# Performance work log

Measured on AMD Instinct MI355X. Metric: run time of the kernel, lower is better.

The kernel has to match this reference:

```python
import jax, jax.numpy as jnp
import numpy as np

EMBED_DIM = 1024
NUM_HEADS = 16
HEAD_DIM = EMBED_DIM // NUM_HEADS


def setup_inputs() -> dict:
    key = jax.random.key(0)
    ks = jax.random.split(key, 10)
    s = 1.0 / np.sqrt(EMBED_DIM)
    inp = {
        "x1": jax.random.normal(ks[0], (4, 1024, EMBED_DIM), jnp.float32),
        "x2": jax.random.normal(ks[1], (4, 2048, EMBED_DIM), jnp.float32),
        "Wq": jax.random.normal(ks[2], (EMBED_DIM, EMBED_DIM), jnp.float32) * s,
        "bq": jnp.zeros((EMBED_DIM,), jnp.float32),
        "Wk": jax.random.normal(ks[3], (EMBED_DIM, EMBED_DIM), jnp.float32) * s,
        "bk": jnp.zeros((EMBED_DIM,), jnp.float32),
        "Wv": jax.random.normal(ks[4], (EMBED_DIM, EMBED_DIM), jnp.float32) * s,
        "bv": jnp.zeros((EMBED_DIM,), jnp.float32),
        "Wo": jax.random.normal(ks[5], (EMBED_DIM, EMBED_DIM), jnp.float32) * s,
        "bo": jnp.zeros((EMBED_DIM,), jnp.float32),
    }
    return inp


def reference(x1, x2, Wq, bq, Wk, bk, Wv, bv, Wo, bo):
    B, Sq, E = x1.shape
    Skv = x2.shape[1]
    H, D = NUM_HEADS, HEAD_DIM
    # linear projections (PyTorch Linear: x @ W.T + b)
    q = (x1 @ Wq.T + bq).reshape(B, Sq, H, D).transpose(0, 2, 1, 3)   # [B,H,Sq,D]
    k = (x2 @ Wk.T + bk).reshape(B, Skv, H, D).transpose(0, 2, 1, 3)  # [B,H,Skv,D]
    v = (x2 @ Wv.T + bv).reshape(B, Skv, H, D).transpose(0, 2, 1, 3)
    scores = jnp.einsum("bhqd,bhkd->bhqk", q, k) / jnp.sqrt(jnp.float32(D))
    attn = jax.nn.softmax(scores, axis=-1)
    out = jnp.einsum("bhqk,bhkd->bhqd", attn, v)
    out = out.transpose(0, 2, 1, 3).reshape(B, Sq, E)
    return out @ Wo.T + bo
```

## Files before the change

### kernel.cpp

```cpp
#include <hip/hip_runtime.h>

typedef __attribute__((ext_vector_type(8))) short short8;
typedef __attribute__((ext_vector_type(4))) short short4v;
typedef __attribute__((ext_vector_type(4))) float f32x4;

#define ASYNC16(g, l) __builtin_amdgcn_global_load_lds( \
    (__attribute__((address_space(1))) void*)(g), \
    (__attribute__((address_space(3))) void*)(l), 16, 0, 0)

__device__ __forceinline__ short f2bf(float f) {
  union { float f; unsigned u; } v; v.f = f;
  unsigned r = v.u + 0x7fffu + ((v.u >> 16) & 1u);
  return (short)(r >> 16);
}

__device__ __forceinline__ unsigned pack_bf2(float lo, float hi) {
  union { float f; unsigned u; } a, b; a.f = lo; b.f = hi;
  return __builtin_amdgcn_perm(b.u + 0x8000u, a.u + 0x8000u, 0x07060302u);
}

__device__ __forceinline__ f32x4 fzero4() {
  f32x4 z; z[0] = 0.f; z[1] = 0.f; z[2] = 0.f; z[3] = 0.f; return z;
}

__device__ __forceinline__ void wg_barrier() {
  asm volatile("s_waitcnt lgkmcnt(0)\n\ts_barrier" ::: "memory");
}

__global__ __launch_bounds__(256) void cvt_all(
    const float* __restrict__ x1, const float* __restrict__ x2,
    const float* __restrict__ wq, const float* __restrict__ wk,
    const float* __restrict__ wv, const float* __restrict__ wo,
    short* __restrict__ dst) {
  long e = ((long)blockIdx.x * 256 + threadIdx.x) * 4;
  const float* src; long loc;
  if (e < 4194304L)       { src = x1; loc = e; }
  else if (e < 12582912L) { src = x2; loc = e - 4194304L; }
  else if (e < 13631488L) { src = wq; loc = e - 12582912L; }
  else if (e < 14680064L) { src = wk; loc = e - 13631488L; }
  else if (e < 15728640L) { src = wv; loc = e - 14680064L; }
  else                    { src = wo; loc = e - 15728640L; }
  float4 v = *(const float4*)(src + loc);
  short4v o;
  o[0] = f2bf(v.x); o[1] = f2bf(v.y); o[2] = f2bf(v.z); o[3] = f2bf(v.w);
  *(short4v*)(dst + e) = o;
}

__global__ __launch_bounds__(256) void proj(
    const short* __restrict__ xb1, const short* __restrict__ xb2,
    const short* __restrict__ wqp, const short* __restrict__ wkp, const short* __restrict__ wvp,
    const float* __restrict__ bq, const float* __restrict__ bk, const float* __restrict__ bv,
    short* __restrict__ qb, short* __restrict__ kb, short* __restrict__ vb) {
  __shared__ short smem[16384];
  short* As = smem;
  short* Bs = smem + 4096;
  const int tid = threadIdx.x, w = tid >> 6, lane = tid & 63;
  const int quad = lane >> 4, col = lane & 15;
  const int waveM = (w >> 1) * 64, waveN = (w & 1) * 64;
  const int my = blockIdx.x, bn = blockIdx.y * 128;
  const short* A; const short* W; const float* bias; int mode, bm;
  if (my < 32)      { A = xb1; W = wqp; bias = bq; mode = 0; bm = my * 128; }
  else if (my < 96) { A = xb2; W = wkp; bias = bk; mode = 1; bm = (my - 32) * 128; }
  else              { A = xb2; W = wvp; bias = bv; mode = 2; bm = (my - 96) * 128; }

  f32x4 acc[4][4];
  for (int mi = 0; mi < 4; ++mi)
    for (int ni = 0; ni < 4; ++ni)
      acc[mi][ni] = fzero4();

  const int srow = w * 16 + (lane >> 2), scol = (lane & 3) * 8;
  const short* ga = A + (size_t)(bm + srow) * 1024 + scol;
  const short* gb = W + (size_t)(bn + srow) * 1024 + scol;
  short* lA = As + w * 512;
  short* lB = Bs + w * 512;

  for (int kk = 0; kk < 1024; kk += 32) {
    __syncthreads();
    ASYNC16(ga + kk,         lA);
    ASYNC16(ga + kk + 65536, lA + 2048);
    ASYNC16(gb + kk,         lB);
    ASYNC16(gb + kk + 65536, lB + 2048);
    __syncthreads();
    short8 af[4], bf[4];
    for (int mi = 0; mi < 4; ++mi)
      af[mi] = *(const short8*)(As + (waveM + mi * 16 + col) * 32 + quad * 8);
    for (int ni = 0; ni < 4; ++ni)
      bf[ni] = *(const short8*)(Bs + (waveN + ni * 16 + col) * 32 + quad * 8);
    for (int mi = 0; mi < 4; ++mi)
      for (int ni = 0; ni < 4; ++ni)
        acc[mi][ni] = __builtin_amdgcn_mfma_f32_16x16x32_bf16(af[mi], bf[ni], acc[mi][ni], 0, 0, 0);
  }

  __syncthreads();
  for (int ni = 0; ni < 4; ++ni) {
    int nn = waveN + ni * 16 + col;
    float bvl = bias[bn + nn];
    for (int mi = 0; mi < 4; ++mi) {
      int m0 = waveM + mi * 16 + quad * 4;
      for (int r = 0; r < 4; ++r) {
        int m = m0 + r;
        smem[m * 128 + (nn ^ ((m & 15) << 3))] = f2bf(acc[mi][ni][r] + bvl);
      }
    }
  }
  __syncthreads();
  if (mode < 2) {
    const int S = (mode == 0) ? 1024 : 2048;
    short* outp = (mode == 0) ? qb : kb;
    const int bb = bm / S, s0 = bm & (S - 1), h0 = bn >> 6;
    for (int it = 0; it < 8; ++it) {
      int f = (it * 256 + tid) * 8;
      int hh = f >> 13, rem = f & 8191, m = rem >> 6, d = rem & 63;
      int nn = hh * 64 + d;
      short8 val = *(const short8*)&smem[m * 128 + (nn ^ ((m & 15) << 3))];
      *(short8*)(outp + ((((size_t)(bb * 16 + h0 + hh)) * S + s0 + m) * 64 + d)) = val;
    }
  } else {
    const int bb = bm >> 11, s0 = bm & 2047, kt0 = s0 >> 6, h0 = bn >> 6;
    for (int it = 0; it < 8; ++it) {
      int f = (it * 256 + tid) * 8;
      int hh = f >> 13, rem = f & 8191, ktl = rem >> 12, r3 = rem & 4095;
      int d = r3 >> 6, kvp0 = r3 & 63;
      int nn = hh * 64 + d;
      short8 val;
      for (int j = 0; j < 8; ++j) {
        int kvp = kvp0 + j;
        int kv = ((kvp & 3) << 4) | (kvp >> 2);
        int m = ktl * 64 + kv;
        val[j] = smem[m * 128 + (nn ^ ((m & 15) << 3))];
      }
      *(short8*)(vb + ((((size_t)(bb * 16 + h0 + hh)) * 32 + (kt0 + ktl)) * 4096) + d * 64 + kvp0) = val;
    }
  }
}

__global__ __launch_bounds__(256) void out_gemm(
    const short* __restrict__ A, const short* __restrict__ W,
    const float* __restrict__ bias, float* __restrict__ out) {
  __shared__ short As[64 * 32];
  __shared__ short Bs[128 * 32];
  const int tid = threadIdx.x, w = tid >> 6, lane = tid & 63;
  const int quad = lane >> 4, col = lane & 15;
  const int waveM = (w >> 1) * 32, waveN = (w & 1) * 64;
  const int bn = blockIdx.x * 128, bm = blockIdx.y * 64;

  f32x4 acc[2][4];
  for (int mi = 0; mi < 2; ++mi)
    for (int ni = 0; ni < 4; ++ni)
      acc[mi][ni] = fzero4();

  const short* ga = A + (size_t)(bm + (tid >> 2)) * 1024 + (tid & 3) * 8;
  const short* gb = W + (size_t)(bn + (tid >> 2)) * 1024 + (tid & 3) * 8;
  short* lA = As + w * 512;
  short* lB = Bs + w * 512;

  for (int kk = 0; kk < 1024; kk += 32) {
    __syncthreads();
    ASYNC16(ga + kk,         lA);
    ASYNC16(gb + kk,         lB);
    ASYNC16(gb + kk + 65536, lB + 2048);
    __syncthreads();
    short8 af[2], bf[4];
    for (int mi = 0; mi < 2; ++mi)
      af[mi] = *(const short8*)(As + (waveM + mi * 16 + col) * 32 + quad * 8);
    for (int ni = 0; ni < 4; ++ni)
      bf[ni] = *(const short8*)(Bs + (waveN + ni * 16 + col) * 32 + quad * 8);
    for (int mi = 0; mi < 2; ++mi)
      for (int ni = 0; ni < 4; ++ni)
        acc[mi][ni] = __builtin_amdgcn_mfma_f32_16x16x32_bf16(af[mi], bf[ni], acc[mi][ni], 0, 0, 0);
  }

  for (int ni = 0; ni < 4; ++ni) {
    int n = bn + waveN + ni * 16 + col;
    float bvl = bias[n];
    for (int mi = 0; mi < 2; ++mi) {
      int m0 = bm + waveM + mi * 16 + quad * 4;
      for (int r = 0; r < 4; ++r)
        out[(size_t)(m0 + r) * 1024 + n] = acc[mi][ni][r] + bvl;
    }
  }
}

__global__ __launch_bounds__(256, 2) void attn(
    const short* __restrict__ Q, const short* __restrict__ K,
    const short* __restrict__ V, short* __restrict__ O) {
  __shared__ short Ks[128 * 72];
  __shared__ short Vs[64 * 136];
  __shared__ short Ps[128 * 136];
  const int tid = threadIdx.x, w = tid >> 6, lane = tid & 63;
  const int quad = lane >> 4, col = lane & 15;
  const int bh = blockIdx.x, qt = blockIdx.y;
  const int b = bh >> 4, h = bh & 15;
  const int qbase = w * 32;

  const short* qp = Q + ((size_t)bh * 1024 + qt * 128) * 64;
  const short* kp = K + (size_t)bh * 131072;
  const short* vp = V + (size_t)bh * 131072;

  short8 aq[2][2];
  for (int mi = 0; mi < 2; ++mi) {
    const short* qr = qp + (qbase + mi * 16 + col) * 64 + quad * 8;
    aq[mi][0] = *(const short8*)qr;
    aq[mi][1] = *(const short8*)(qr + 32);
  }

  float lsum[2][4];
  f32x4 oa[2][4];
  for (int mi = 0; mi < 2; ++mi) {
    for (int r = 0; r < 4; ++r) lsum[mi][r] = 0.f;
    for (int ni = 0; ni < 4; ++ni) oa[mi][ni] = fzero4();
  }

  const int krow = lane + (w >> 1) * 64, kch = (w & 1) * 32;
  const int vd = lane, vch = w & 1, vkh = (w >> 1) * 32;
  const float c = 0.18033688011112042f;

  short8 kpre[4], vpre[4];
  {
    const short* kg = kp + krow * 64 + kch;
    const short* vg = vp + vch * 4096 + vd * 64 + vkh;
    for (int i = 0; i < 4; ++i) kpre[i] = *(const short8*)(kg + i * 8);
    for (int i = 0; i < 4; ++i) vpre[i] = *(const short8*)(vg + i * 8);
  }

  for (int kt = 0; kt < 16; ++kt) {
    wg_barrier();
    for (int i = 0; i < 4; ++i)
      *(short8*)&Ks[krow * 72 + kch + i * 8] = kpre[i];
    for (int i = 0; i < 4; ++i)
      *(short8*)&Vs[vd * 136 + vch * 64 + vkh + i * 8] = vpre[i];
    {
      int ktn = (kt < 15) ? kt + 1 : kt;
      const short* kg = kp + ktn * 8192 + krow * 64 + kch;
      const short* vg = vp + (2 * ktn + vch) * 4096 + vd * 64 + vkh;
      for (int i = 0; i < 4; ++i) kpre[i] = *(const short8*)(kg + i * 8);
      for (int i = 0; i < 4; ++i) vpre[i] = *(const short8*)(vg + i * 8);
    }
    wg_barrier();

    for (int mi = 0; mi < 2; ++mi) {
      f32x4 sf[8];
      for (int nk = 0; nk < 8; ++nk) {
        short8 bk0 = *(const short8*)&Ks[(nk * 16 + col) * 72 + quad * 8];
        short8 bk1 = *(const short8*)&Ks[(nk * 16 + col) * 72 + 32 + quad * 8];
        f32x4 z = fzero4();
        z = __builtin_amdgcn_mfma_f32_16x16x32_bf16(aq[mi][0], bk0, z, 0, 0, 0);
        z = __builtin_amdgcn_mfma_f32_16x16x32_bf16(aq[mi][1], bk1, z, 0, 0, 0);
        sf[nk] = z;
      }
      for (int nk = 0; nk < 8; ++nk)
        for (int r = 0; r < 4; ++r)
          sf[nk][r] = __builtin_amdgcn_exp2f(sf[nk][r] * c);
      for (int r = 0; r < 4; ++r)
        lsum[mi][r] += ((sf[0][r] + sf[1][r]) + (sf[2][r] + sf[3][r])) +
                       ((sf[4][r] + sf[5][r]) + (sf[6][r] + sf[7][r]));
      for (int r = 0; r < 4; ++r) {
        int row = qbase + mi * 16 + quad * 4 + r;
        uint2 d0, d1;
        d0.x = pack_bf2(sf[0][r], sf[1][r]);
        d0.y = pack_bf2(sf[2][r], sf[3][r]);
        d1.x = pack_bf2(sf[4][r], sf[5][r]);
        d1.y = pack_bf2(sf[6][r], sf[7][r]);
        *(uint2*)&Ps[row * 136 + col * 4]      = d0;
        *(uint2*)&Ps[row * 136 + 64 + col * 4] = d1;
      }
    }

    for (int ks = 0; ks < 4; ++ks) {
      int koff = ks * 32 + quad * 8;
      short8 ap0 = *(const short8*)&Ps[(qbase + col) * 136 + koff];
      short8 ap1 = *(const short8*)&Ps[(qbase + 16 + col) * 136 + koff];
      for (int ni = 0; ni < 4; ++ni) {
        short8 bv = *(const short8*)&Vs[(ni * 16 + col) * 136 + koff];
        oa[0][ni] = __builtin_amdgcn_mfma_f32_16x16x32_bf16(ap0, bv, oa[0][ni], 0, 0, 0);
        oa[1][ni] = __builtin_amdgcn_mfma_f32_16x16x32_bf16(ap1, bv, oa[1][ni], 0, 0, 0);
      }
    }
  }

  for (int mi = 0; mi < 2; ++mi)
    for (int r = 0; r < 4; ++r) {
      float s = lsum[mi][r];
      s += __shfl_xor(s, 1);
      s += __shfl_xor(s, 2);
      s += __shfl_xor(s, 4);
      s += __shfl_xor(s, 8);
      lsum[mi][r] = 1.f / s;
    }
  __syncthreads();
  for (int mi = 0; mi < 2; ++mi)
    for (int ni = 0; ni < 4; ++ni)
      for (int r = 0; r < 4; ++r)
        Ps[(qbase + mi * 16 + quad * 4 + r) * 64 + ni * 16 + col] = f2bf(oa[mi][ni][r] * lsum[mi][r]);
  __syncthreads();
  for (int it = 0; it < 4; ++it) {
    int f = (it * 256 + tid) * 8;
    int q = f >> 6, d = f & 63;
    short8 val = *(const short8*)&Ps[q * 64 + d];
    *(short8*)(O + ((size_t)(b * 1024 + qt * 128 + q)) * 1024 + h * 64 + d) = val;
  }
}

extern "C" void kernel_launch(void* const* d_in, const int* in_sizes, int n_in,
                              void* d_out, int out_size, void* d_ws, size_t ws_size,
                              hipStream_t stream) {
  const float* x1 = (const float*)d_in[0];
  const float* x2 = (const float*)d_in[1];
  const float* Wq = (const float*)d_in[2];
  const float* bq = (const float*)d_in[3];
  const float* Wk = (const float*)d_in[4];
  const float* bk = (const float*)d_in[5];
  const float* Wv = (const float*)d_in[6];
  const float* bv = (const float*)d_in[7];
  const float* Wo = (const float*)d_in[8];
  const float* bo = (const float*)d_in[9];

  char* ws = (char*)d_ws;
  short* xb1 = (short*)(ws + 0);
  short* xb2 = (short*)(ws + 8388608);
  short* wqb = (short*)(ws + 25165824);
  short* wkb = (short*)(ws + 27262976);
  short* wvb = (short*)(ws + 29360128);
  short* wob = (short*)(ws + 31457280);
  short* qb  = (short*)(ws + 33554432);
  short* kb  = (short*)(ws + 41943040);
  short* vb  = (short*)(ws + 58720256);
  short* ob  = (short*)(ws + 75497472);

  cvt_all<<<16384, 256, 0, stream>>>(x1, x2, Wq, Wk, Wv, Wo, (short*)ws);
  proj<<<dim3(160, 8), 256, 0, stream>>>(xb1, xb2, wqb, wkb, wvb, bq, bk, bv, qb, kb, vb);
  attn<<<dim3(64, 8), 256, 0, stream>>>(qb, kb, vb, ob);
  out_gemm<<<dim3(8, 64), 256, 0, stream>>>(ob, wob, bo, (float*)d_out);
}
```

Baseline: 246.2 us.

## Fold softmax scale into Q, use fp16 P/V with row-sum MFMA column, retile out GEMM

```diff
diff --git a/kernel.cpp b/kernel.cpp
--- a/kernel.cpp
+++ b/kernel.cpp
@@ -3,6 +3,7 @@
 typedef __attribute__((ext_vector_type(8))) short short8;
 typedef __attribute__((ext_vector_type(4))) short short4v;
 typedef __attribute__((ext_vector_type(4))) float f32x4;
+typedef _Float16 half8 __attribute__((ext_vector_type(8)));
 
 #define ASYNC16(g, l) __builtin_amdgcn_global_load_lds( \
     (__attribute__((address_space(1))) void*)(g), \
@@ -14,9 +15,13 @@
   return (short)(r >> 16);
 }
 
-__device__ __forceinline__ unsigned pack_bf2(float lo, float hi) {
-  union { float f; unsigned u; } a, b; a.f = lo; b.f = hi;
-  return __builtin_amdgcn_perm(b.u + 0x8000u, a.u + 0x8000u, 0x07060302u);
+__device__ __forceinline__ short f2h(float f) {
+  _Float16 h = (_Float16)f;
+  return __builtin_bit_cast(short, h);
+}
+
+__device__ __forceinline__ unsigned pkh2(float a, float b) {
+  return __builtin_bit_cast(unsigned, __builtin_amdgcn_cvt_pkrtz(a, b));
 }
 
 __device__ __forceinline__ f32x4 fzero4() {
@@ -99,7 +104,12 @@
       int m0 = waveM + mi * 16 + quad * 4;
       for (int r = 0; r < 4; ++r) {
         int m = m0 + r;
-        smem[m * 128 + (nn ^ ((m & 15) << 3))] = f2bf(acc[mi][ni][r] + bvl);
+        float val = acc[mi][ni][r] + bvl;
+        short sv;
+        if (mode == 0)      sv = f2bf(val * 0.18033688011112042f);
+        else if (mode == 1) sv = f2bf(val);
+        else                sv = f2h(val);
+        smem[m * 128 + (nn ^ ((m & 15) << 3))] = sv;
       }
     }
   }
@@ -137,43 +147,51 @@
 __global__ __launch_bounds__(256) void out_gemm(
     const short* __restrict__ A, const short* __restrict__ W,
     const float* __restrict__ bias, float* __restrict__ out) {
-  __shared__ short As[64 * 32];
-  __shared__ short Bs[128 * 32];
+  __shared__ short As[2][4096];
+  __shared__ short Bs[2][2048];
   const int tid = threadIdx.x, w = tid >> 6, lane = tid & 63;
   const int quad = lane >> 4, col = lane & 15;
-  const int waveM = (w >> 1) * 32, waveN = (w & 1) * 64;
-  const int bn = blockIdx.x * 128, bm = blockIdx.y * 64;
-
-  f32x4 acc[2][4];
-  for (int mi = 0; mi < 2; ++mi)
-    for (int ni = 0; ni < 4; ++ni)
+  const int waveM = (w >> 1) * 64, waveN = (w & 1) * 32;
+  const int bn = blockIdx.x * 64, bm = blockIdx.y * 128;
+
+  f32x4 acc[4][2];
+  for (int mi = 0; mi < 4; ++mi)
+    for (int ni = 0; ni < 2; ++ni)
       acc[mi][ni] = fzero4();
 
-  const short* ga = A + (size_t)(bm + (tid >> 2)) * 1024 + (tid & 3) * 8;
+  const int arow = w * 16 + (lane >> 2), ac = (lane & 3) * 8;
+  const short* ga = A + (size_t)(bm + arow) * 1024 + ac;
   const short* gb = W + (size_t)(bn + (tid >> 2)) * 1024 + (tid & 3) * 8;
-  short* lA = As + w * 512;
-  short* lB = Bs + w * 512;
-
-  for (int kk = 0; kk < 1024; kk += 32) {
+  short* lA0 = As[0] + w * 512; short* lA1 = As[1] + w * 512;
+  short* lB0 = Bs[0] + w * 512; short* lB1 = Bs[1] + w * 512;
+
+  for (int kk = 0; kk < 1024; kk += 64) {
     __syncthreads();
-    ASYNC16(ga + kk,         lA);
-    ASYNC16(gb + kk,         lB);
-    ASYNC16(gb + kk + 65536, lB + 2048);
+    ASYNC16(ga + kk,              lA0);
+    ASYNC16(ga + kk + 65536,      lA0 + 2048);
+    ASYNC16(ga + kk + 32,         lA1);
+    ASYNC16(ga + kk + 32 + 65536, lA1 + 2048);
+    ASYNC16(gb + kk,              lB0);
+    ASYNC16(gb + kk + 32,         lB1);
     __syncthreads();
-    short8 af[2], bf[4];
-    for (int mi = 0; mi < 2; ++mi)
-      af[mi] = *(const short8*)(As + (waveM + mi * 16 + col) * 32 + quad * 8);
-    for (int ni = 0; ni < 4; ++ni)
-      bf[ni] = *(const short8*)(Bs + (waveN + ni * 16 + col) * 32 + quad * 8);
-    for (int mi = 0; mi < 2; ++mi)
-      for (int ni = 0; ni < 4; ++ni)
-        acc[mi][ni] = __builtin_amdgcn_mfma_f32_16x16x32_bf16(af[mi], bf[ni], acc[mi][ni], 0, 0, 0);
-  }
-
-  for (int ni = 0; ni < 4; ++ni) {
+    for (int kh = 0; kh < 2; ++kh) {
+      const short* Ash = As[kh];
+      const short* Bsh = Bs[kh];
+      short8 af[4], bf[2];
+      for (int mi = 0; mi < 4; ++mi)
+        af[mi] = *(const short8*)(Ash + (waveM + mi * 16 + col) * 32 + quad * 8);
+      for (int ni = 0; ni < 2; ++ni)
+        bf[ni] = *(const short8*)(Bsh + (waveN + ni * 16 + col) * 32 + quad * 8);
+      for (int mi = 0; mi < 4; ++mi)
+        for (int ni = 0; ni < 2; ++ni)
+          acc[mi][ni] = __builtin_amdgcn_mfma_f32_16x16x32_bf16(af[mi], bf[ni], acc[mi][ni], 0, 0, 0);
+    }
+  }
+
+  for (int ni = 0; ni < 2; ++ni) {
     int n = bn + waveN + ni * 16 + col;
     float bvl = bias[n];
-    for (int mi = 0; mi < 2; ++mi) {
+    for (int mi = 0; mi < 4; ++mi) {
       int m0 = bm + waveM + mi * 16 + quad * 4;
       for (int r = 0; r < 4; ++r)
         out[(size_t)(m0 + r) * 1024 + n] = acc[mi][ni][r] + bvl;
@@ -185,7 +203,7 @@
     const short* __restrict__ Q, const short* __restrict__ K,
     const short* __restrict__ V, short* __restrict__ O) {
   __shared__ short Ks[128 * 72];
-  __shared__ short Vs[64 * 136];
+  __shared__ short Vs[80 * 136];
   __shared__ short Ps[128 * 136];
   const int tid = threadIdx.x, w = tid >> 6, lane = tid & 63;
   const int quad = lane >> 4, col = lane & 15;
@@ -204,16 +222,16 @@
     aq[mi][1] = *(const short8*)(qr + 32);
   }
 
-  float lsum[2][4];
-  f32x4 oa[2][4];
-  for (int mi = 0; mi < 2; ++mi) {
-    for (int r = 0; r < 4; ++r) lsum[mi][r] = 0.f;
-    for (int ni = 0; ni < 4; ++ni) oa[mi][ni] = fzero4();
-  }
+  f32x4 oa[2][5];
+  for (int mi = 0; mi < 2; ++mi)
+    for (int ni = 0; ni < 5; ++ni)
+      oa[mi][ni] = fzero4();
+
+  for (int i = tid; i < 16 * 136; i += 256)
+    Vs[64 * 136 + i] = (i < 136) ? (short)0x3C00 : (short)0;
 
   const int krow = lane + (w >> 1) * 64, kch = (w & 1) * 32;
   const int vd = lane, vch = w & 1, vkh = (w >> 1) * 32;
-  const float c = 0.18033688011112042f;
 
   short8 kpre[4], vpre[4];
   {
@@ -238,60 +256,58 @@
     }
     wg_barrier();
 
-    for (int mi = 0; mi < 2; ++mi) {
-      f32x4 sf[8];
-      for (int nk = 0; nk < 8; ++nk) {
-        short8 bk0 = *(const short8*)&Ks[(nk * 16 + col) * 72 + quad * 8];
-        short8 bk1 = *(const short8*)&Ks[(nk * 16 + col) * 72 + 32 + quad * 8];
-        f32x4 z = fzero4();
-        z = __builtin_amdgcn_mfma_f32_16x16x32_bf16(aq[mi][0], bk0, z, 0, 0, 0);
-        z = __builtin_amdgcn_mfma_f32_16x16x32_bf16(aq[mi][1], bk1, z, 0, 0, 0);
-        sf[nk] = z;
-      }
+    f32x4 sf[2][8];
+    for (int nk = 0; nk < 8; ++nk) {
+      short8 bk0 = *(const short8*)&Ks[(nk * 16 + col) * 72 + quad * 8];
+      short8 bk1 = *(const short8*)&Ks[(nk * 16 + col) * 72 + 32 + quad * 8];
+      f32x4 z0 = fzero4(), z1 = fzero4();
+      z0 = __builtin_amdgcn_mfma_f32_16x16x32_bf16(aq[0][0], bk0, z0, 0, 0, 0);
+      z0 = __builtin_amdgcn_mfma_f32_16x16x32_bf16(aq[0][1], bk1, z0, 0, 0, 0);
+      z1 = __builtin_amdgcn_mfma_f32_16x16x32_bf16(aq[1][0], bk0, z1, 0, 0, 0);
+      z1 = __builtin_amdgcn_mfma_f32_16x16x32_bf16(aq[1][1], bk1, z1, 0, 0, 0);
+      sf[0][nk] = z0;
+      sf[1][nk] = z1;
+    }
+
+    for (int mi = 0; mi < 2; ++mi)
       for (int nk = 0; nk < 8; ++nk)
         for (int r = 0; r < 4; ++r)
-          sf[nk][r] = __builtin_amdgcn_exp2f(sf[nk][r] * c);
-      for (int r = 0; r < 4; ++r)
-        lsum[mi][r] += ((sf[0][r] + sf[1][r]) + (sf[2][r] + sf[3][r])) +
-                       ((sf[4][r] + sf[5][r]) + (sf[6][r] + sf[7][r]));
+          sf[mi][nk][r] = __builtin_amdgcn_exp2f(sf[mi][nk][r]);
+    for (int mi = 0; mi < 2; ++mi)
       for (int r = 0; r < 4; ++r) {
         int row = qbase + mi * 16 + quad * 4 + r;
         uint2 d0, d1;
-        d0.x = pack_bf2(sf[0][r], sf[1][r]);
-        d0.y = pack_bf2(sf[2][r], sf[3][r]);
-        d1.x = pack_bf2(sf[4][r], sf[5][r]);
-        d1.y = pack_bf2(sf[6][r], sf[7][r]);
+        d0.x = pkh2(sf[mi][0][r], sf[mi][1][r]);
+        d0.y = pkh2(sf[mi][2][r], sf[mi][3][r]);
+        d1.x = pkh2(sf[mi][4][r], sf[mi][5][r]);
+        d1.y = pkh2(sf[mi][6][r], sf[mi][7][r]);
         *(uint2*)&Ps[row * 136 + col * 4]      = d0;
         *(uint2*)&Ps[row * 136 + 64 + col * 4] = d1;
       }
-    }
 
     for (int ks = 0; ks < 4; ++ks) {
       int koff = ks * 32 + quad * 8;
-      short8 ap0 = *(const short8*)&Ps[(qbase + col) * 136 + koff];
-      short8 ap1 = *(const short8*)&Ps[(qbase + 16 + col) * 136 + koff];
-      for (int ni = 0; ni < 4; ++ni) {
-        short8 bv = *(const short8*)&Vs[(ni * 16 + col) * 136 + koff];
-        oa[0][ni] = __builtin_amdgcn_mfma_f32_16x16x32_bf16(ap0, bv, oa[0][ni], 0, 0, 0);
-        oa[1][ni] = __builtin_amdgcn_mfma_f32_16x16x32_bf16(ap1, bv, oa[1][ni], 0, 0, 0);
+      half8 ap0 = *(const half8*)&Ps[(qbase + col) * 136 + koff];
+      half8 ap1 = *(const half8*)&Ps[(qbase + 16 + col) * 136 + koff];
+      for (int ni = 0; ni < 5; ++ni) {
+        half8 bv = *(const half8*)&Vs[(ni * 16 + col) * 136 + koff];
+        oa[0][ni] = __builtin_amdgcn_mfma_f32_16x16x32_f16(ap0, bv, oa[0][ni], 0, 0, 0);
+        oa[1][ni] = __builtin_amdgcn_mfma_f32_16x16x32_f16(ap1, bv, oa[1][ni], 0, 0, 0);
       }
     }
   }
 
+  float inv[2][4];
   for (int mi = 0; mi < 2; ++mi)
     for (int r = 0; r < 4; ++r) {
-      float s = lsum[mi][r];
-      s += __shfl_xor(s, 1);
-      s += __shfl_xor(s, 2);
-      s += __shfl_xor(s, 4);
-      s += __shfl_xor(s, 8);
-      lsum[mi][r] = 1.f / s;
+      float s = __shfl(oa[mi][4][r], lane & 48);
+      inv[mi][r] = 1.f / s;
     }
   __syncthreads();
   for (int mi = 0; mi < 2; ++mi)
     for (int ni = 0; ni < 4; ++ni)
       for (int r = 0; r < 4; ++r)
-        Ps[(qbase + mi * 16 + quad * 4 + r) * 64 + ni * 16 + col] = f2bf(oa[mi][ni][r] * lsum[mi][r]);
+        Ps[(qbase + mi * 16 + quad * 4 + r) * 64 + ni * 16 + col] = f2bf(oa[mi][ni][r] * inv[mi][r]);
   __syncthreads();
   for (int it = 0; it < 4; ++it) {
     int f = (it * 256 + tid) * 8;
@@ -330,5 +346,5 @@
   cvt_all<<<16384, 256, 0, stream>>>(x1, x2, Wq, Wk, Wv, Wo, (short*)ws);
   proj<<<dim3(160, 8), 256, 0, stream>>>(xb1, xb2, wqb, wkb, wvb, bq, bk, bv, qb, kb, vb);
   attn<<<dim3(64, 8), 256, 0, stream>>>(qb, kb, vb, ob);
-  out_gemm<<<dim3(8, 64), 256, 0, stream>>>(ob, wob, bo, (float*)d_out);
-}
+  out_gemm<<<dim3(16, 32), 256, 0, stream>>>(ob, wob, bo, (float*)d_out);
+}
```

Measured after the change: 240.6 us. -2.3%, faster.
